# Kernel tuning notes

Hardware: AMD Instinct MI355X
Metric: run time of the kernel (lower is better)

The kernel has to match this reference:

```python
import jax, jax.numpy as jnp
import numpy as np

B = 131072      # batch size
H = 300         # hidden_dim (per-source), se has 2*H = 600 columns
T = 2           # num_source_tasks
EPS = 1e-20


def setup_inputs() -> dict:
    key = jax.random.key(0)
    k1, k2, k3, k4, k5 = jax.random.split(key, 5)
    return {
        "se1": jax.random.normal(k1, (B, H), dtype=jnp.float32),
        "se2": jax.random.normal(k2, (B, H), dtype=jnp.float32),
        "W": jax.random.normal(k3, (T, 2 * H), dtype=jnp.float32) / np.sqrt(2 * H).astype(np.float32),
        "b": jax.random.normal(k4, (T,), dtype=jnp.float32),
        "u": jax.random.uniform(k5, (B, T), dtype=jnp.float32),
        "n_tasks": 2,
    }


def reference(se1, se2, W, b, u, n_tasks):
    # se = torch.cat(se, dim=1) -> [B, 2H]
    se = jnp.concatenate([se1, se2], axis=1)
    # tiny linear + relu + log_softmax
    se_postrelu = jax.nn.relu(se @ W.T + b)            # [B, T]
    logits = jax.nn.log_softmax(se_postrelu, axis=1)   # [B, T]
    # straight-through gumbel-softmax (temperature=1.0, no mask)
    gumbel = -jnp.log(-jnp.log(u + EPS) + EPS)
    y = jax.nn.softmax(logits + gumbel, axis=1)        # soft probs
    y_hard = jax.nn.one_hot(jnp.argmax(y, axis=1), T, dtype=y.dtype)
    selector = jax.lax.stop_gradient(y_hard - y) + y   # ST estimator, [B, T]
    # rf: first H cols = selector[:,0], next H cols = selector[:,1]
    rf = jnp.repeat(selector, H, axis=1)               # [B, 2H]
    return se * rf
```

## Files before the change

### kernel.cpp

```cpp
#include <hip/hip_runtime.h>
#include <math.h>

typedef float f4 __attribute__((ext_vector_type(4)));

#define BDIM 256
#define TROWS 8
#define TILE_F4_IN 600
#define TILE_F4_OUT 1200

__device__ __forceinline__ float dot4(f4 a, f4 w) {
    return a[0]*w[0] + a[1]*w[1] + a[2]*w[2] + a[3]*w[3];
}

__global__ __launch_bounds__(BDIM, 6) void taskselector_kernel(
    const f4* __restrict__ se1,
    const f4* __restrict__ se2,
    const float* __restrict__ W,
    const float* __restrict__ bvec,
    const f4* __restrict__ u4,
    f4* __restrict__ out)
{
    __shared__ f4 L1[TILE_F4_IN];
    __shared__ f4 L2[TILE_F4_IN];
    __shared__ float SEL[TROWS * 2];
    __shared__ f4 UL[TROWS / 2];

    const int tid  = threadIdx.x;
    const int lane = tid & 63;
    const int wave = tid >> 6;
    const int tile = blockIdx.x;

    const f4* s1 = se1 + (size_t)tile * TILE_F4_IN;
    const f4* s2 = se2 + (size_t)tile * TILE_F4_IN;
    const f4 zero = (f4)0.f;
    const bool t3 = (tid < TILE_F4_IN - 2 * BDIM);
    f4 t0 = __builtin_nontemporal_load(s1 + tid);
    f4 t1 = __builtin_nontemporal_load(s1 + BDIM + tid);
    f4 t2 = t3 ? __builtin_nontemporal_load(s1 + 2 * BDIM + tid) : zero;
    f4 q0 = __builtin_nontemporal_load(s2 + tid);
    f4 q1 = __builtin_nontemporal_load(s2 + BDIM + tid);
    f4 q2 = t3 ? __builtin_nontemporal_load(s2 + 2 * BDIM + tid) : zero;
    if (tid < TROWS / 2) UL[tid] = u4[(size_t)tile * (TROWS / 2) + tid];

    const bool extra = (lane < 11);
    const f4* W0 = (const f4*)W;
    const f4* W1 = (const f4*)(W + 600);
    f4 w0a = W0[lane];
    f4 w0b = extra ? W0[64 + lane]  : zero;
    f4 w0c = W0[75 + lane];
    f4 w0d = extra ? W0[139 + lane] : zero;
    f4 w1a = W1[lane];
    f4 w1b = extra ? W1[64 + lane]  : zero;
    f4 w1c = W1[75 + lane];
    f4 w1d = extra ? W1[139 + lane] : zero;
    const float b0 = bvec[0];
    const float b1 = bvec[1];

    L1[tid] = t0;
    L1[BDIM + tid] = t1;
    L2[tid] = q0;
    L2[BDIM + tid] = q1;
    if (t3) {
        L1[2 * BDIM + tid] = t2;
        L2[2 * BDIM + tid] = q2;
    }
    __syncthreads();

    const float* ULf = (const float*)UL;
    #pragma unroll
    for (int rr = 0; rr < 2; rr++) {
        const int r = wave * 2 + rr;
        const f4* R1 = L1 + r * 75;
        const f4* R2 = L2 + r * 75;
        f4 a0 = R1[lane];
        f4 c0 = R2[lane];
        f4 a1 = extra ? R1[64 + lane] : zero;
        f4 c1 = extra ? R2[64 + lane] : zero;
        float d0 = dot4(a0, w0a) + dot4(a1, w0b) + dot4(c0, w0c) + dot4(c1, w0d);
        float d1 = dot4(a0, w1a) + dot4(a1, w1b) + dot4(c0, w1c) + dot4(c1, w1d);
        #pragma unroll
        for (int off = 32; off > 0; off >>= 1) {
            d0 += __shfl_xor(d0, off, 64);
            d1 += __shfl_xor(d1, off, 64);
        }
        float z0 = fmaxf(d0 + b0, 0.f);
        float z1 = fmaxf(d1 + b1, 0.f);
        float m  = fmaxf(z0, z1);
        float lse = m + logf(expf(z0 - m) + expf(z1 - m));
        float uu0 = ULf[2 * r];
        float uu1 = ULf[2 * r + 1];
        float q0v = (z0 - lse) + (-logf(-logf(uu0 + 1e-20f) + 1e-20f));
        float q1v = (z1 - lse) + (-logf(-logf(uu1 + 1e-20f) + 1e-20f));
        float mm = fmaxf(q0v, q1v);
        float e0 = expf(q0v - mm);
        float e1 = expf(q1v - mm);
        float s  = e0 + e1;
        float y0 = e0 / s;
        float y1 = e1 / s;
        bool  pick0 = (q0v >= q1v);
        float s0 = pick0 ? ((1.f - y0) + y0) : 0.f;
        float s1v = pick0 ? 0.f : ((1.f - y1) + y1);
        if (lane == 0) { SEL[2 * r] = s0; SEL[2 * r + 1] = s1v; }
    }
    __syncthreads();

    f4* o = out + (size_t)tile * TILE_F4_OUT;
    #pragma unroll
    for (int k = 0; k < 4; k++) {
        const int j   = k * BDIM + tid;
        const int row = j / 150;
        const int rem = j - row * 150;
        const bool first = (rem < 75);
        f4 v = first ? L1[row * 75 + rem] : L2[row * 75 + rem - 75];
        float sc = SEL[2 * row + (first ? 0 : 1)];
        __builtin_nontemporal_store(v * sc, o + j);
    }
    if (tid < TILE_F4_OUT - 4 * BDIM) {
        const int j   = 4 * BDIM + tid;
        const int row = j / 150;
        const int rem = j - row * 150;
        const bool first = (rem < 75);
        f4 v = first ? L1[row * 75 + rem] : L2[row * 75 + rem - 75];
        float sc = SEL[2 * row + (first ? 0 : 1)];
        __builtin_nontemporal_store(v * sc, o + j);
    }
}

extern "C" void kernel_launch(void* const* d_in, const int* in_sizes, int n_in,
                              void* d_out, int out_size, void* d_ws, size_t ws_size,
                              hipStream_t stream) {
    const f4* se1 = (const f4*)d_in[0];
    const f4* se2 = (const f4*)d_in[1];
    const float* W = (const float*)d_in[2];
    const float* b = (const float*)d_in[3];
    const f4* u4  = (const f4*)d_in[4];
    f4* out = (f4*)d_out;

    const int Brows = in_sizes[0] / 300;
    const int ntiles = Brows / TROWS;

    taskselector_kernel<<<ntiles, BDIM, 0, stream>>>(se1, se2, W, b, u4, out);
}
```

Baseline: 110.1 us.

## Convert to persistent grid with register-prefetched double-buffered tiles

Replaces the one-block-per-tile launch with a fixed grid of 1024 persistent blocks that loop over tiles. The next tile is loaded into registers while the current one is processed, and shared memory is double-buffered. The goal is to overlap global loads with compute and stores, and to avoid paying block launch and weight load costs for every tile. In exchange, the grid has fewer blocks, so memory-level parallelism may drop, and the kernel uses more LDS and registers, lowering occupancy (launch bounds drop from 6 to 4). It also assumes the tile count divides evenly by 1024.

```diff
diff --git a/kernel.cpp b/kernel.cpp
--- a/kernel.cpp
+++ b/kernel.cpp
@@ -7,40 +7,31 @@
 #define TROWS 8
 #define TILE_F4_IN 600
 #define TILE_F4_OUT 1200
+#define NBLK 1024
 
 __device__ __forceinline__ float dot4(f4 a, f4 w) {
     return a[0]*w[0] + a[1]*w[1] + a[2]*w[2] + a[3]*w[3];
 }
 
-__global__ __launch_bounds__(BDIM, 6) void taskselector_kernel(
+__global__ __launch_bounds__(BDIM, 4) void taskselector_kernel(
     const f4* __restrict__ se1,
     const f4* __restrict__ se2,
     const float* __restrict__ W,
     const float* __restrict__ bvec,
     const f4* __restrict__ u4,
-    f4* __restrict__ out)
+    f4* __restrict__ out,
+    int ntiles)
 {
-    __shared__ f4 L1[TILE_F4_IN];
-    __shared__ f4 L2[TILE_F4_IN];
-    __shared__ float SEL[TROWS * 2];
-    __shared__ f4 UL[TROWS / 2];
+    __shared__ f4 L1[2][TILE_F4_IN];
+    __shared__ f4 L2[2][TILE_F4_IN];
+    __shared__ float SEL[2][TROWS * 2];
+    __shared__ f4 UL[2][TROWS / 2];
 
     const int tid  = threadIdx.x;
     const int lane = tid & 63;
     const int wave = tid >> 6;
-    const int tile = blockIdx.x;
-
-    const f4* s1 = se1 + (size_t)tile * TILE_F4_IN;
-    const f4* s2 = se2 + (size_t)tile * TILE_F4_IN;
+    const bool t3  = (tid < TILE_F4_IN - 2 * BDIM);
     const f4 zero = (f4)0.f;
-    const bool t3 = (tid < TILE_F4_IN - 2 * BDIM);
-    f4 t0 = __builtin_nontemporal_load(s1 + tid);
-    f4 t1 = __builtin_nontemporal_load(s1 + BDIM + tid);
-    f4 t2 = t3 ? __builtin_nontemporal_load(s1 + 2 * BDIM + tid) : zero;
-    f4 q0 = __builtin_nontemporal_load(s2 + tid);
-    f4 q1 = __builtin_nontemporal_load(s2 + BDIM + tid);
-    f4 q2 = t3 ? __builtin_nontemporal_load(s2 + 2 * BDIM + tid) : zero;
-    if (tid < TROWS / 2) UL[tid] = u4[(size_t)tile * (TROWS / 2) + tid];
 
     const bool extra = (lane < 11);
     const f4* W0 = (const f4*)W;
@@ -56,73 +47,109 @@
     const float b0 = bvec[0];
     const float b1 = bvec[1];
 
-    L1[tid] = t0;
-    L1[BDIM + tid] = t1;
-    L2[tid] = q0;
-    L2[BDIM + tid] = q1;
-    if (t3) {
-        L1[2 * BDIM + tid] = t2;
-        L2[2 * BDIM + tid] = q2;
+    const int nit = ntiles / NBLK;
+
+    int tile = blockIdx.x;
+    f4 rt0, rt1, rt2, rq0, rq1, rq2, ru;
+    {
+        const f4* s1 = se1 + (size_t)tile * TILE_F4_IN;
+        const f4* s2 = se2 + (size_t)tile * TILE_F4_IN;
+        rt0 = __builtin_nontemporal_load(s1 + tid);
+        rt1 = __builtin_nontemporal_load(s1 + BDIM + tid);
+        rt2 = t3 ? __builtin_nontemporal_load(s1 + 2 * BDIM + tid) : zero;
+        rq0 = __builtin_nontemporal_load(s2 + tid);
+        rq1 = __builtin_nontemporal_load(s2 + BDIM + tid);
+        rq2 = t3 ? __builtin_nontemporal_load(s2 + 2 * BDIM + tid) : zero;
+        ru  = (tid < TROWS / 2) ? u4[(size_t)tile * (TROWS / 2) + tid] : zero;
     }
-    __syncthreads();
 
-    const float* ULf = (const float*)UL;
-    #pragma unroll
-    for (int rr = 0; rr < 2; rr++) {
-        const int r = wave * 2 + rr;
-        const f4* R1 = L1 + r * 75;
-        const f4* R2 = L2 + r * 75;
-        f4 a0 = R1[lane];
-        f4 c0 = R2[lane];
-        f4 a1 = extra ? R1[64 + lane] : zero;
-        f4 c1 = extra ? R2[64 + lane] : zero;
-        float d0 = dot4(a0, w0a) + dot4(a1, w0b) + dot4(c0, w0c) + dot4(c1, w0d);
-        float d1 = dot4(a0, w1a) + dot4(a1, w1b) + dot4(c0, w1c) + dot4(c1, w1d);
+    for (int it = 0; it < nit; ++it) {
+        const int cur = it & 1;
+
+        L1[cur][tid] = rt0;
+        L1[cur][BDIM + tid] = rt1;
+        L2[cur][tid] = rq0;
+        L2[cur][BDIM + tid] = rq1;
+        if (t3) {
+            L1[cur][2 * BDIM + tid] = rt2;
+            L2[cur][2 * BDIM + tid] = rq2;
+        }
+        if (tid < TROWS / 2) UL[cur][tid] = ru;
+        __syncthreads();
+
+        if (it + 1 < nit) {
+            const int ntile = tile + NBLK;
+            const f4* s1 = se1 + (size_t)ntile * TILE_F4_IN;
+            const f4* s2 = se2 + (size_t)ntile * TILE_F4_IN;
+            rt0 = __builtin_nontemporal_load(s1 + tid);
+            rt1 = __builtin_nontemporal_load(s1 + BDIM + tid);
+            if (t3) rt2 = __builtin_nontemporal_load(s1 + 2 * BDIM + tid);
+            rq0 = __builtin_nontemporal_load(s2 + tid);
+            rq1 = __builtin_nontemporal_load(s2 + BDIM + tid);
+            if (t3) rq2 = __builtin_nontemporal_load(s2 + 2 * BDIM + tid);
+            if (tid < TROWS / 2) ru = u4[(size_t)ntile * (TROWS / 2) + tid];
+        }
+
+        const float* ULf = (const float*)&UL[cur][0];
         #pragma unroll
-        for (int off = 32; off > 0; off >>= 1) {
-            d0 += __shfl_xor(d0, off, 64);
-            d1 += __shfl_xor(d1, off, 64);
+        for (int rr = 0; rr < 2; rr++) {
+            const int r = wave * 2 + rr;
+            const f4* R1 = &L1[cur][0] + r * 75;
+            const f4* R2 = &L2[cur][0] + r * 75;
+            f4 a0 = R1[lane];
+            f4 c0 = R2[lane];
+            f4 a1 = extra ? R1[64 + lane] : zero;
+            f4 c1 = extra ? R2[64 + lane] : zero;
+            float d0 = dot4(a0, w0a) + dot4(a1, w0b) + dot4(c0, w0c) + dot4(c1, w0d);
+            float d1 = dot4(a0, w1a) + dot4(a1, w1b) + dot4(c0, w1c) + dot4(c1, w1d);
+            #pragma unroll
+            for (int off = 32; off > 0; off >>= 1) {
+                d0 += __shfl_xor(d0, off, 64);
+                d1 += __shfl_xor(d1, off, 64);
+            }
+            float z0 = fmaxf(d0 + b0, 0.f);
+            float z1 = fmaxf(d1 + b1, 0.f);
+            float m  = fmaxf(z0, z1);
+            float lse = m + logf(expf(z0 - m) + expf(z1 - m));
+            float uu0 = ULf[2 * r];
+            float uu1 = ULf[2 * r + 1];
+            float q0v = (z0 - lse) + (-logf(-logf(uu0 + 1e-20f) + 1e-20f));
+            float q1v = (z1 - lse) + (-logf(-logf(uu1 + 1e-20f) + 1e-20f));
+            float mm = fmaxf(q0v, q1v);
+            float e0 = expf(q0v - mm);
+            float e1 = expf(q1v - mm);
+            float s  = e0 + e1;
+            float y0 = e0 / s;
+            float y1 = e1 / s;
+            bool  pick0 = (q0v >= q1v);
+            float s0 = pick0 ? ((1.f - y0) + y0) : 0.f;
+            float s1v = pick0 ? 0.f : ((1.f - y1) + y1);
+            if (lane == 0) { SEL[cur][2 * r] = s0; SEL[cur][2 * r + 1] = s1v; }
         }
-        float z0 = fmaxf(d0 + b0, 0.f);
-        float z1 = fmaxf(d1 + b1, 0.f);
-        float m  = fmaxf(z0, z1);
-        float lse = m + logf(expf(z0 - m) + expf(z1 - m));
-        float uu0 = ULf[2 * r];
-        float uu1 = ULf[2 * r + 1];
-        float q0v = (z0 - lse) + (-logf(-logf(uu0 + 1e-20f) + 1e-20f));
-        float q1v = (z1 - lse) + (-logf(-logf(uu1 + 1e-20f) + 1e-20f));
-        float mm = fmaxf(q0v, q1v);
-        float e0 = expf(q0v - mm);
-        float e1 = expf(q1v - mm);
-        float s  = e0 + e1;
-        float y0 = e0 / s;
-        float y1 = e1 / s;
-        bool  pick0 = (q0v >= q1v);
-        float s0 = pick0 ? ((1.f - y0) + y0) : 0.f;
-        float s1v = pick0 ? 0.f : ((1.f - y1) + y1);
-        if (lane == 0) { SEL[2 * r] = s0; SEL[2 * r + 1] = s1v; }
-    }
-    __syncthreads();
+        __syncthreads();
 
-    f4* o = out + (size_t)tile * TILE_F4_OUT;
-    #pragma unroll
-    for (int k = 0; k < 4; k++) {
-        const int j   = k * BDIM + tid;
-        const int row = j / 150;
-        const int rem = j - row * 150;
-        const bool first = (rem < 75);
-        f4 v = first ? L1[row * 75 + rem] : L2[row * 75 + rem - 75];
-        float sc = SEL[2 * row + (first ? 0 : 1)];
-        __builtin_nontemporal_store(v * sc, o + j);
-    }
-    if (tid < TILE_F4_OUT - 4 * BDIM) {
-        const int j   = 4 * BDIM + tid;
-        const int row = j / 150;
-        const int rem = j - row * 150;
-        const bool first = (rem < 75);
-        f4 v = first ? L1[row * 75 + rem] : L2[row * 75 + rem - 75];
-        float sc = SEL[2 * row + (first ? 0 : 1)];
-        __builtin_nontemporal_store(v * sc, o + j);
+        f4* o = out + (size_t)tile * TILE_F4_OUT;
+        #pragma unroll
+        for (int k = 0; k < 4; k++) {
+            const int j   = k * BDIM + tid;
+            const int row = j / 150;
+            const int rem = j - row * 150;
+            const bool first = (rem < 75);
+            f4 v = first ? L1[cur][row * 75 + rem] : L2[cur][row * 75 + rem - 75];
+            float sc = SEL[cur][2 * row + (first ? 0 : 1)];
+            __builtin_nontemporal_store(v * sc, o + j);
+        }
+        if (tid < TILE_F4_OUT - 4 * BDIM) {
+            const int j   = 4 * BDIM + tid;
+            const int row = j / 150;
+            const int rem = j - row * 150;
+            const bool first = (rem < 75);
+            f4 v = first ? L1[cur][row * 75 + rem] : L2[cur][row * 75 + rem - 75];
+            float sc = SEL[cur][2 * row + (first ? 0 : 1)];
+            __builtin_nontemporal_store(v * sc, o + j);
+        }
+
+        tile += NBLK;
     }
 }
 
@@ -139,5 +166,5 @@
     const int Brows = in_sizes[0] / 300;
     const int ntiles = Brows / TROWS;
 
-    taskselector_kernel<<<ntiles, BDIM, 0, stream>>>(se1, se2, W, b, u4, out);
+    taskselector_kernel<<<NBLK, BDIM, 0, stream>>>(se1, se2, W, b, u4, out, ntiles);
 }
```

New measurement: 122.8 us. 1.12x slower.
